# Performance work log

Measured on AMD Instinct MI355X. Metric: run time of the kernel, lower is better.

## Reference

```python
import jax, jax.numpy as jnp
import numpy as np

L, B, E = 2048, 4, 1024
H = 8
D1 = 2048          # expand_ratio * E, multiple of H
HD = D1 // H       # head dim 256
MAX_L = 2048
EPS = 1e-8


def setup_inputs() -> dict:
    key = jax.random.key(0)
    ks = jax.random.split(key, 9)
    std = 0.02
    return {
        "x": jax.random.normal(ks[0], (L, B, E), jnp.float32),
        "Wu": jax.random.normal(ks[1], (D1, E), jnp.float32) * std,
        "bu": jax.random.normal(ks[2], (D1,), jnp.float32) * std,
        "Wv": jax.random.normal(ks[3], (D1, E), jnp.float32) * std,
        "bv": jax.random.normal(ks[4], (D1,), jnp.float32) * std,
        "Wo": jax.random.normal(ks[5], (E, D1), jnp.float32) * std,
        "bo": jax.random.normal(ks[6], (E,), jnp.float32) * std,
        "zero": jax.random.normal(ks[7], (H, 1), jnp.float32) * 0.1,   # Toeplitz coef, offset 0
        "pos": jax.random.normal(ks[8], (H, MAX_L - 1), jnp.float32) * 0.1,  # offsets 1..n-1
    }


def _simple_rmsnorm(x):
    d = x.shape[-1]
    rms = jnp.linalg.norm(x, axis=-1, keepdims=True) * (d ** -0.5)
    return x / (rms + EPS)


def _toeplitz_causal_fft(v, zero, pos):
    # v: (b, h, n, hd); causal Toeplitz mixing along n via FFT long conv
    n = v.shape[-2]
    coef = jnp.concatenate([zero, pos[:, : n - 1]], axis=-1)  # (h, n)
    m = 2 * n
    cf = jnp.fft.rfft(coef, m, axis=-1)                  # (h, m//2+1)
    vf = jnp.fft.rfft(v, m, axis=-2)                     # (b, h, m//2+1, hd)
    out = jnp.fft.irfft(cf[None, :, :, None] * vf, m, axis=-2)
    return out[:, :, :n, :]


def reference(x, Wu, bu, Wv, bv, Wo, bo, zero, pos):
    # x: (n, b, e) fairseq layout
    n, b, e = x.shape
    shortcut = x
    xn = _simple_rmsnorm(x)                               # pre_norm (SimpleRMSNorm, no params)
    u = jax.nn.silu(jnp.einsum('nbe,de->nbd', xn, Wu) + bu)   # (n,b,d1)
    v = jax.nn.silu(jnp.einsum('nbe,de->nbd', xn, Wv) + bv)   # (n,b,d1)
    # 'n b (h d) -> b h n d'
    vh = v.transpose(1, 0, 2).reshape(b, n, H, HD).transpose(0, 2, 1, 3)
    oh = _toeplitz_causal_fft(vh, zero, pos)              # (b,h,n,hd)
    o = oh.transpose(0, 2, 1, 3).reshape(b, n, D1).transpose(1, 0, 2)  # (n,b,d1)
    o = u * o                                             # gating
    out = jnp.einsum('nbd,ed->nbe', o, Wo) + bo + shortcut
    return out
```

## Files before the change

### kernel.cpp

```cpp
#include <hip/hip_runtime.h>
#include <cstdint>
#include <cstddef>

#define LQ   2048
#define BQ   4
#define EQ   1024
#define HQ   8
#define D1Q  2048
#define HDQ  256
#define NBQ  (LQ*BQ)

typedef __bf16 bf16_t;
typedef __bf16 bf16x8 __attribute__((ext_vector_type(8)));
typedef __bf16 bf16x4 __attribute__((ext_vector_type(4)));
typedef float  f32x4  __attribute__((ext_vector_type(4)));

#define GAS1(p) ((const __attribute__((address_space(1))) void*)(p))
#define LAS3(p) ((__attribute__((address_space(3))) void*)(p))


__global__ __launch_bounds__(256) void convert_kernel(
    const float* __restrict__ Wu, const float* __restrict__ Wv,
    const float* __restrict__ Wo,
    bf16_t* __restrict__ Wub, bf16_t* __restrict__ Wvb,
    bf16_t* __restrict__ Wob)
{
    const size_t i = (size_t)blockIdx.x * 256 + threadIdx.x;
    if (i < (size_t)D1Q * EQ) {
        Wub[i] = (bf16_t)Wu[i];
        Wvb[i] = (bf16_t)Wv[i];
        Wob[i] = (bf16_t)Wo[i];
    }
}

__global__ __launch_bounds__(256) void build_toep_tiles(
    const float* __restrict__ zero, const float* __restrict__ pos,
    bf16_t* __restrict__ Atiles)
{
    const int q = blockIdx.x;
    const int h = blockIdx.y;
    const int doff = (q - 3) * 32;
    const int tid = threadIdx.x;
    bf16_t* dst = Atiles + ((size_t)h * 64 + q) * (128 * 32);
    const int e0 = tid * 16;
    const int r = e0 >> 5;
    const int cbase = e0 & 31;
    bf16_t vals[16];
    #pragma unroll
    for (int j = 0; j < 16; ++j) {
        const int d = doff + r - (cbase + j);
        float v = 0.f;
        if (d == 0) v = zero[h];
        else if (d > 0) v = pos[(size_t)h * (LQ - 1) + d - 1];
        vals[j] = (bf16_t)v;
    }
    *(bf16x8*)(dst + e0)     = *(bf16x8*)(vals);
    *(bf16x8*)(dst + e0 + 8) = *(bf16x8*)(vals + 8);
}

__global__ __launch_bounds__(256) void rmsnorm_kernel(
    const float* __restrict__ x, bf16_t* __restrict__ xn)
{
    const int row = blockIdx.x;
    const int tid = threadIdx.x;
    const float4 v = ((const float4*)(x + (size_t)row * EQ))[tid];
    float ss = v.x*v.x + v.y*v.y + v.z*v.z + v.w*v.w;
    #pragma unroll
    for (int m = 32; m >= 1; m >>= 1) ss += __shfl_xor(ss, m, 64);
    __shared__ float red[4];
    const int wid = tid >> 6, lane = tid & 63;
    if (lane == 0) red[wid] = ss;
    __syncthreads();
    const float tot = red[0] + red[1] + red[2] + red[3];
    const float inv = 1.f / (sqrtf(tot * (1.f / EQ)) + 1e-8f);
    bf16x4 o;
    o[0] = (bf16_t)(v.x * inv); o[1] = (bf16_t)(v.y * inv);
    o[2] = (bf16_t)(v.z * inv); o[3] = (bf16_t)(v.w * inv);
    *(bf16x4*)(xn + (size_t)row * EQ + tid * 4) = o;
}


template<int NREP, int MODE>
__global__ __launch_bounds__(512, 1) void gemm8p(
    const bf16_t* __restrict__ A, const bf16_t* __restrict__ Bm,
    int K, int N,
    const float* __restrict__ bias, const float* __restrict__ res,
    bf16_t* __restrict__ Cb, float* __restrict__ Cf)
{
    constexpr int LB      = NREP / 2;
    constexpr int BSTRIDE = 16384 + NREP * 4096;
    __shared__ alignas(16) char smem[3 * BSTRIDE];

    const int nwg   = gridDim.x * gridDim.y;
    const int bid   = blockIdx.y * gridDim.x + blockIdx.x;
    const int chunkw = nwg >> 3;
    const int sb    = (bid & 7) * chunkw + (bid >> 3);
    const int bx    = sb % gridDim.x;
    const int by    = sb / gridDim.x;

    const int tid  = threadIdx.x;
    const int wid  = tid >> 6;
    const int lane = tid & 63;
    const int frow = lane & 15;
    const int c    = lane >> 4;
    const int m0 = by * 256;
    const int n0 = bx * (NREP * 64);
    const int wrm = (wid >> 2) * 128;
    const int wrn = (wid & 3) * (NREP * 16);

    const int Ra = wrm + frow;
    const int ga = (Ra ^ (Ra >> 2)) & 3;
    const int offA = Ra * 64 + ((c ^ ga) << 4);
    const int Rb = wrn + frow;
    const int gb = (Rb ^ (Rb >> 2)) & 3;
    const int offB = 16384 + Rb * 64 + ((c ^ gb) << 4);

    const int sr   = tid >> 2;
    const int slot = tid & 3;
    const int gs   = (sr ^ (sr >> 2)) & 3;
    const size_t lda = (size_t)K * 2;
    const char* srcA  = (const char*)A  + (size_t)(m0 + sr) * lda + ((slot ^ gs) << 4);
    const char* srcA2 = srcA + 128 * lda;
    const char* srcB  = (const char*)Bm + (size_t)(n0 + sr) * lda + ((slot ^ gs) << 4);
    const char* srcB2 = srcB + 128 * lda;

    auto STAGE_A = [&](int buf, int kt) {
        char* d = smem + buf * BSTRIDE + wid * 1024;
        __builtin_amdgcn_global_load_lds(GAS1(srcA  + (size_t)kt * 64), LAS3(d), 16, 0, 0);
        __builtin_amdgcn_global_load_lds(GAS1(srcA2 + (size_t)kt * 64), LAS3(d + 8192), 16, 0, 0);
    };
    auto STAGE_B = [&](int buf, int kt) {
        char* d = smem + buf * BSTRIDE + 16384 + wid * 1024;
        __builtin_amdgcn_global_load_lds(GAS1(srcB  + (size_t)kt * 64), LAS3(d), 16, 0, 0);
        if constexpr (LB == 2)
            __builtin_amdgcn_global_load_lds(GAS1(srcB2 + (size_t)kt * 64), LAS3(d + 8192), 16, 0, 0);
    };

    f32x4 acc[8][NREP];
    #pragma unroll
    for (int i = 0; i < 8; ++i)
        #pragma unroll
        for (int j = 0; j < NREP; ++j) acc[i][j] = (f32x4){0.f, 0.f, 0.f, 0.f};

    const int NT = K >> 5;

    STAGE_A(0, 0); STAGE_B(0, 0);
    STAGE_A(1, 1); STAGE_B(1, 1);
    if constexpr (LB == 2) asm volatile("s_waitcnt vmcnt(4)" ::: "memory");
    else                   asm volatile("s_waitcnt vmcnt(3)" ::: "memory");
    __builtin_amdgcn_s_barrier();

    int buf = 0;
    for (int kq = 0; kq < NT; ++kq) {
        const char* base = smem + buf * BSTRIDE;
        int pbuf = buf + 2; if (pbuf >= 3) pbuf -= 3;
        const bool pf = (kq < NT - 2);

        bf16x8 av[4], bv[NREP];
        #pragma unroll
        for (int i = 0; i < 4; ++i)
            av[i] = *(const bf16x8*)(base + offA + i * 1024);
        #pragma unroll
        for (int i = 0; i < NREP; ++i)
            bv[i] = *(const bf16x8*)(base + offB + i * 1024);
        if (pf) STAGE_A(pbuf, kq + 2);
        __builtin_amdgcn_s_barrier();
        __builtin_amdgcn_s_setprio(1);
        #pragma unroll
        for (int mi = 0; mi < 4; ++mi)
            #pragma unroll
            for (int ni = 0; ni < NREP; ++ni)
                acc[mi][ni] = __builtin_amdgcn_mfma_f32_16x16x32_bf16(
                    av[mi], bv[ni], acc[mi][ni], 0, 0, 0);
        __builtin_amdgcn_s_setprio(0);
        __builtin_amdgcn_sched_barrier(0);
        __builtin_amdgcn_s_barrier();

        #pragma unroll
        for (int i = 0; i < 4; ++i)
            av[i] = *(const bf16x8*)(base + offA + (4 + i) * 1024);
        if (pf) STAGE_B(pbuf, kq + 2);
        __builtin_amdgcn_s_barrier();
        __builtin_amdgcn_s_setprio(1);
        #pragma unroll
        for (int mi = 0; mi < 4; ++mi)
            #pragma unroll
            for (int ni = 0; ni < NREP; ++ni)
                acc[4 + mi][ni] = __builtin_amdgcn_mfma_f32_16x16x32_bf16(
                    av[mi], bv[ni], acc[4 + mi][ni], 0, 0, 0);
        __builtin_amdgcn_s_setprio(0);
        __builtin_amdgcn_sched_barrier(0);

        if (kq < NT - 1) {
            if (kq <= NT - 3) {
                if constexpr (LB == 2) asm volatile("s_waitcnt vmcnt(4)" ::: "memory");
                else                   asm volatile("s_waitcnt vmcnt(3)" ::: "memory");
            } else {
                asm volatile("s_waitcnt vmcnt(0)" ::: "memory");
            }
            __builtin_amdgcn_s_barrier();
        }
        buf = (buf == 2) ? 0 : buf + 1;
    }

    if constexpr (MODE == 1) {
        static_assert(NREP == 4, "MODE 1 requires NREP=4");
        const int hh = n0 >> 8;
        float bb[4];
        #pragma unroll
        for (int ni = 0; ni < 4; ++ni) bb[ni] = bias[n0 + wrn + ni * 16 + frow];

        #pragma unroll
        for (int p = 0; p < 2; ++p) {
            __syncthreads();
            bf16_t* chunk = (bf16_t*)smem + wid * 4608;
            #pragma unroll
            for (int mi2 = 0; mi2 < 4; ++mi2) {
                #pragma unroll
                for (int ni = 0; ni < 4; ++ni) {
                    const int nl = ni * 16 + frow;
                    #pragma unroll
                    for (int j = 0; j < 4; ++j) {
                        float v = acc[p * 4 + mi2][ni][j] + bb[ni];
                        v = v / (1.f + __expf(-v));
                        chunk[nl * 72 + j * 16 + mi2 * 4 + c] = (bf16_t)v;
                    }
                }
            }
            __syncthreads();
            const int hd = wrn + lane;
            const int tb = (m0 + wrm + p * 64) >> 2;
            const bf16_t* rowp = chunk + lane * 72;
            #pragma unroll
            for (int b2 = 0; b2 < 4; ++b2) {
                bf16x8 r0 = *(const bf16x8*)(rowp + b2 * 16);
                bf16x8 r1 = *(const bf16x8*)(rowp + b2 * 16 + 8);
                bf16_t* dst = Cb + (((size_t)hh * 4 + b2) * 256 + hd) * (size_t)LQ + tb;
                *(bf16x8*)(dst)     = r0;
                *(bf16x8*)(dst + 8) = r1;
            }
        }
        return;
    }

    const int fq = c * 4;
    #pragma unroll
    for (int mi = 0; mi < 8; ++mi) {
        #pragma unroll
        for (int ni = 0; ni < NREP; ++ni) {
            const int gn = n0 + wrn + ni * 16 + frow;
            #pragma unroll
            for (int j = 0; j < 4; ++j) {
                const int gm = m0 + wrm + mi * 16 + fq + j;
                float v = acc[mi][ni][j];
                if constexpr (MODE == 0) {
                    v += bias[gn];
                    v = v / (1.f + __expf(-v));
                    Cb[(size_t)gm * N + gn] = (bf16_t)v;
                } else {
                    v += bias[gn] + res[(size_t)gm * N + gn];
                    Cf[(size_t)gm * N + gn] = v;
                }
            }
        }
    }
}

__global__ __launch_bounds__(512, 4) void gemm_toep8p(
    const bf16_t* __restrict__ VT, const bf16_t* __restrict__ Atiles,
    const bf16_t* __restrict__ U, bf16_t* __restrict__ O)
{
    constexpr int BSTRIDE = 24576;
    __shared__ alignas(16) char smem[3 * BSTRIDE];

    const int bid   = blockIdx.x;
    const int m_blk = 15 - (bid >> 5);
    const int sub   = bid & 31;
    const int h     = sub >> 2;
    const int n0    = (sub & 3) * 256;
    const int m0    = m_blk * 128;

    const int tid  = threadIdx.x;
    const int wid  = tid >> 6;
    const int lane = tid & 63;
    const int frow = lane & 15;
    const int c    = lane >> 4;
    const int wrm  = (wid >> 2) * 64;
    const int wrn  = (wid & 3) * 64;

    const int Ra = wrm + frow;
    const int ga = (Ra ^ (Ra >> 2)) & 3;
    const int offA = Ra * 64 + ((c ^ ga) << 4);
    const int Rb = wrn + frow;
    const int gb = (Rb ^ (Rb >> 2)) & 3;
    const int offB = 8192 + Rb * 64 + ((c ^ gb) << 4);

    const int sr   = tid >> 2;
    const int slot = tid & 3;
    const int gs   = (sr ^ (sr >> 2)) & 3;
    const int soff = (slot ^ gs) << 4;

    const char* Ah = (const char*)(Atiles + (size_t)h * 64 * 4096);
    const size_t ldb = (size_t)LQ * 2;
    const char* srcB  = (const char*)VT + ((size_t)h * 1024 + n0 + sr) * ldb + soff;
    const char* srcB2 = srcB + 128 * ldb;

    auto STAGE_A = [&](int buf, int kt) {
        const int q = 4 * m_blk + 3 - kt;
        const char* s = Ah + (size_t)q * 8192 + (size_t)sr * 64 + soff;
        __builtin_amdgcn_global_load_lds(GAS1(s),
                                         LAS3(smem + buf * BSTRIDE + wid * 1024), 16, 0, 0);
    };
    auto STAGE_B = [&](int buf, int kt) {
        char* d = smem + buf * BSTRIDE + 8192 + wid * 1024;
        __builtin_amdgcn_global_load_lds(GAS1(srcB  + (size_t)kt * 64), LAS3(d), 16, 0, 0);
        __builtin_amdgcn_global_load_lds(GAS1(srcB2 + (size_t)kt * 64), LAS3(d + 8192), 16, 0, 0);
    };

    f32x4 acc[4][4];
    #pragma unroll
    for (int i = 0; i < 4; ++i)
        #pragma unroll
        for (int j = 0; j < 4; ++j) acc[i][j] = (f32x4){0.f, 0.f, 0.f, 0.f};

    const int NT = 4 * m_blk + 4;

    STAGE_A(0, 0); STAGE_B(0, 0);
    STAGE_A(1, 1); STAGE_B(1, 1);
    asm volatile("s_waitcnt vmcnt(3)" ::: "memory");
    __builtin_amdgcn_s_barrier();

    int buf = 0;
    for (int kq = 0; kq < NT; ++kq) {
        const char* base = smem + buf * BSTRIDE;
        int pbuf = buf + 2; if (pbuf >= 3) pbuf -= 3;
        const bool pf = (kq < NT - 2);

        bf16x8 av[4], bv[4];
        #pragma unroll
        for (int i = 0; i < 4; ++i)
            av[i] = *(const bf16x8*)(base + offA + i * 1024);
        #pragma unroll
        for (int i = 0; i < 2; ++i)
            bv[i] = *(const bf16x8*)(base + offB + i * 1024);
        if (pf) STAGE_A(pbuf, kq + 2);
        __builtin_amdgcn_s_barrier();
        __builtin_amdgcn_s_setprio(1);
        #pragma unroll
        for (int mi = 0; mi < 4; ++mi)
            #pragma unroll
            for (int ni = 0; ni < 2; ++ni)
                acc[mi][ni] = __builtin_amdgcn_mfma_f32_16x16x32_bf16(
                    av[mi], bv[ni], acc[mi][ni], 0, 0, 0);
        __builtin_amdgcn_s_setprio(0);
        __builtin_amdgcn_sched_barrier(0);
        __builtin_amdgcn_s_barrier();

        #pragma unroll
        for (int i = 2; i < 4; ++i)
            bv[i] = *(const bf16x8*)(base + offB + i * 1024);
        if (pf) STAGE_B(pbuf, kq + 2);
        __builtin_amdgcn_s_barrier();
        __builtin_amdgcn_s_setprio(1);
        #pragma unroll
        for (int mi = 0; mi < 4; ++mi)
            #pragma unroll
            for (int ni = 2; ni < 4; ++ni)
                acc[mi][ni] = __builtin_amdgcn_mfma_f32_16x16x32_bf16(
                    av[mi], bv[ni], acc[mi][ni], 0, 0, 0);
        __builtin_amdgcn_s_setprio(0);
        __builtin_amdgcn_sched_barrier(0);

        if (kq < NT - 1) {
            if (kq <= NT - 3) asm volatile("s_waitcnt vmcnt(3)" ::: "memory");
            else              asm volatile("s_waitcnt vmcnt(0)" ::: "memory");
            __builtin_amdgcn_s_barrier();
        }
        buf = (buf == 2) ? 0 : buf + 1;
    }

    const int fq = c * 4;
    #pragma unroll
    for (int mi = 0; mi < 4; ++mi) {
        #pragma unroll
        for (int ni = 0; ni < 4; ++ni) {
            const int nn = n0 + wrn + ni * 16 + frow;
            const int b  = nn >> 8, hd = nn & 255;
            #pragma unroll
            for (int j = 0; j < 4; ++j) {
                const int t = m0 + wrm + mi * 16 + fq + j;
                const size_t idx = ((size_t)t * BQ + b) * D1Q + h * HDQ + hd;
                const float uval = (float)U[idx];
                O[idx] = (bf16_t)(uval * acc[mi][ni][j]);
            }
        }
    }
}


extern "C" void kernel_launch(void* const* d_in, const int* in_sizes, int n_in,
                              void* d_out, int out_size, void* d_ws, size_t ws_size,
                              hipStream_t stream)
{
    const float* x    = (const float*)d_in[0];
    const float* Wu   = (const float*)d_in[1];
    const float* bu   = (const float*)d_in[2];
    const float* Wv   = (const float*)d_in[3];
    const float* bv   = (const float*)d_in[4];
    const float* Wo   = (const float*)d_in[5];
    const float* bo   = (const float*)d_in[6];
    const float* zero = (const float*)d_in[7];
    const float* pos  = (const float*)d_in[8];
    float* out = (float*)d_out;

    char* ws = (char*)d_ws;
    size_t off = 0;
    auto alloc = [&](size_t bytes) {
        char* p = ws + off;
        off += (bytes + 255) & ~(size_t)255;
        return p;
    };
    bf16_t* xn     = (bf16_t*)alloc((size_t)NBQ * EQ * 2);
    bf16_t* Wub    = (bf16_t*)alloc((size_t)D1Q * EQ * 2);
    bf16_t* Wvb    = (bf16_t*)alloc((size_t)D1Q * EQ * 2);
    bf16_t* Wob    = (bf16_t*)alloc((size_t)EQ * D1Q * 2);
    bf16_t* Atiles = (bf16_t*)alloc((size_t)HQ * 64 * 4096 * 2);
    bf16_t* Ub     = (bf16_t*)alloc((size_t)NBQ * D1Q * 2);
    bf16_t* VTb    = (bf16_t*)alloc((size_t)NBQ * D1Q * 2);
    bf16_t* Ob     = (bf16_t*)alloc((size_t)NBQ * D1Q * 2);

    convert_kernel<<<8192, 256, 0, stream>>>(Wu, Wv, Wo, Wub, Wvb, Wob);
    build_toep_tiles<<<dim3(64, 8), 256, 0, stream>>>(zero, pos, Atiles);
    rmsnorm_kernel<<<NBQ, 256, 0, stream>>>(x, xn);

    dim3 g1(D1Q / 256, NBQ / 256);
    gemm8p<4, 0><<<g1, 512, 0, stream>>>(xn, Wub, EQ, D1Q, bu, nullptr, Ub, nullptr);
    gemm8p<4, 1><<<g1, 512, 0, stream>>>(xn, Wvb, EQ, D1Q, bv, nullptr, VTb, nullptr);

    gemm_toep8p<<<512, 512, 0, stream>>>(VTb, Atiles, Ub, Ob);

    dim3 g2(EQ / 128, NBQ / 256);
    gemm8p<2, 2><<<g2, 512, 0, stream>>>(Ob, Wob, D1Q, EQ, bo, x, nullptr, out);
}
```

Before: 225.6 us.

## Restructure GEMM pipeline to double-buffered BK=64 with templated warp geometry

Reworks the dense GEMM kernel from a triple-buffered BK=32 pipeline to a double-buffered BK=64 pipeline with an 8-way XOR swizzle and 128-byte rows. Warp tiling becomes a template (MI, WM, WN), and launch bounds are raised to allow two workgroups per CU. The transposed-store epilogue is rewritten for the new tile layout. The aim is fewer barriers per unit of K and better latency hiding through occupancy. The cost is a shallower prefetch distance and more registers per workgroup. It also drops the sched_barrier calls in the Toeplitz GEMM.

Result: faster. 208.5 us (-7.6%).

```diff
diff --git a/kernel.cpp b/kernel.cpp
--- a/kernel.cpp
+++ b/kernel.cpp
@@ -80,16 +80,24 @@
 }
 
 
-template<int NREP, int MODE>
-__global__ __launch_bounds__(512, 1) void gemm8p(
+template<int MI, int WM, int WN, int MODE>
+__global__ __launch_bounds__(512, 2) void gemm8p(
     const bf16_t* __restrict__ A, const bf16_t* __restrict__ Bm,
     int K, int N,
     const float* __restrict__ bias, const float* __restrict__ res,
     bf16_t* __restrict__ Cb, float* __restrict__ Cf)
 {
-    constexpr int LB      = NREP / 2;
-    constexpr int BSTRIDE = 16384 + NREP * 4096;
-    __shared__ alignas(16) char smem[3 * BSTRIDE];
+    constexpr int BM = WM * MI * 16;
+    constexpr int BN = WN * 64;
+    constexpr int ABYTES = BM * 128;
+    constexpr int BBYTES = BN * 128;
+    constexpr int BSTRIDE = ABYTES + BBYTES;
+    constexpr int CA = BM / 64;
+    constexpr int CB = BN / 64;
+    constexpr int NPH = 2 * (MI / 4);
+    static_assert(BM == 256, "staging assumes BM=256");
+    static_assert(MODE != 1 || (MI == 8 && WN == 4), "MODE1 geometry");
+    __shared__ alignas(16) char smem[2 * BSTRIDE];
 
     const int nwg   = gridDim.x * gridDim.y;
     const int bid   = blockIdx.y * gridDim.x + blockIdx.x;
@@ -103,108 +111,97 @@
     const int lane = tid & 63;
     const int frow = lane & 15;
     const int c    = lane >> 4;
-    const int m0 = by * 256;
-    const int n0 = bx * (NREP * 64);
-    const int wrm = (wid >> 2) * 128;
-    const int wrn = (wid & 3) * (NREP * 16);
-
-    const int Ra = wrm + frow;
-    const int ga = (Ra ^ (Ra >> 2)) & 3;
-    const int offA = Ra * 64 + ((c ^ ga) << 4);
-    const int Rb = wrn + frow;
-    const int gb = (Rb ^ (Rb >> 2)) & 3;
-    const int offB = 16384 + Rb * 64 + ((c ^ gb) << 4);
-
-    const int sr   = tid >> 2;
-    const int slot = tid & 3;
-    const int gs   = (sr ^ (sr >> 2)) & 3;
-    const size_t lda = (size_t)K * 2;
-    const char* srcA  = (const char*)A  + (size_t)(m0 + sr) * lda + ((slot ^ gs) << 4);
-    const char* srcA2 = srcA + 128 * lda;
-    const char* srcB  = (const char*)Bm + (size_t)(n0 + sr) * lda + ((slot ^ gs) << 4);
-    const char* srcB2 = srcB + 128 * lda;
-
-    auto STAGE_A = [&](int buf, int kt) {
-        char* d = smem + buf * BSTRIDE + wid * 1024;
-        __builtin_amdgcn_global_load_lds(GAS1(srcA  + (size_t)kt * 64), LAS3(d), 16, 0, 0);
-        __builtin_amdgcn_global_load_lds(GAS1(srcA2 + (size_t)kt * 64), LAS3(d + 8192), 16, 0, 0);
+    const int m0 = by * BM;
+    const int n0 = bx * BN;
+    const int wm = wid / WN, wn = wid % WN;
+    const int wrm = wm * (MI * 16);
+    const int wrn = wn * 64;
+
+    const int g = frow & 7;
+    const int offA0 = (wrm + frow) * 128 + ((c ^ g) << 4);
+    const int offA1 = offA0 ^ 64;
+    const int offB0 = (wrn + frow) * 128 + ((c ^ g) << 4);
+    const int offB1 = offB0 ^ 64;
+
+    const int rl = tid >> 3;
+    const int ps = tid & 7;
+    const int ls = ps ^ (rl & 7);
+    const size_t lda2 = (size_t)K * 2;
+    const char* sA = (const char*)A  + (size_t)(m0 + rl) * lda2 + ls * 16;
+    const char* sB = (const char*)Bm + (size_t)(n0 + rl) * lda2 + ls * 16;
+
+    auto STAGE_A = [&](int bf, int kt) {
+        char* d = smem + bf * BSTRIDE + wid * 1024;
+        #pragma unroll
+        for (int cl = 0; cl < CA; ++cl)
+            __builtin_amdgcn_global_load_lds(
+                GAS1(sA + (size_t)cl * 64 * lda2 + (size_t)kt * 128),
+                LAS3(d + cl * 8192), 16, 0, 0);
     };
-    auto STAGE_B = [&](int buf, int kt) {
-        char* d = smem + buf * BSTRIDE + 16384 + wid * 1024;
-        __builtin_amdgcn_global_load_lds(GAS1(srcB  + (size_t)kt * 64), LAS3(d), 16, 0, 0);
-        if constexpr (LB == 2)
-            __builtin_amdgcn_global_load_lds(GAS1(srcB2 + (size_t)kt * 64), LAS3(d + 8192), 16, 0, 0);
+    auto STAGE_B = [&](int bf, int kt) {
+        char* d = smem + bf * BSTRIDE + ABYTES + wid * 1024;
+        #pragma unroll
+        for (int cl = 0; cl < CB; ++cl)
+            __builtin_amdgcn_global_load_lds(
+                GAS1(sB + (size_t)cl * 64 * lda2 + (size_t)kt * 128),
+                LAS3(d + cl * 8192), 16, 0, 0);
     };
 
-    f32x4 acc[8][NREP];
-    #pragma unroll
-    for (int i = 0; i < 8; ++i)
-        #pragma unroll
-        for (int j = 0; j < NREP; ++j) acc[i][j] = (f32x4){0.f, 0.f, 0.f, 0.f};
-
-    const int NT = K >> 5;
+    f32x4 acc[MI][4];
+    #pragma unroll
+    for (int i = 0; i < MI; ++i)
+        #pragma unroll
+        for (int j = 0; j < 4; ++j) acc[i][j] = (f32x4){0.f, 0.f, 0.f, 0.f};
+
+    const int NT = K >> 6;
 
     STAGE_A(0, 0); STAGE_B(0, 0);
-    STAGE_A(1, 1); STAGE_B(1, 1);
-    if constexpr (LB == 2) asm volatile("s_waitcnt vmcnt(4)" ::: "memory");
-    else                   asm volatile("s_waitcnt vmcnt(3)" ::: "memory");
+    asm volatile("s_waitcnt vmcnt(0)" ::: "memory");
     __builtin_amdgcn_s_barrier();
 
     int buf = 0;
-    for (int kq = 0; kq < NT; ++kq) {
-        const char* base = smem + buf * BSTRIDE;
-        int pbuf = buf + 2; if (pbuf >= 3) pbuf -= 3;
-        const bool pf = (kq < NT - 2);
-
-        bf16x8 av[4], bv[NREP];
-        #pragma unroll
-        for (int i = 0; i < 4; ++i)
-            av[i] = *(const bf16x8*)(base + offA + i * 1024);
-        #pragma unroll
-        for (int i = 0; i < NREP; ++i)
-            bv[i] = *(const bf16x8*)(base + offB + i * 1024);
-        if (pf) STAGE_A(pbuf, kq + 2);
-        __builtin_amdgcn_s_barrier();
-        __builtin_amdgcn_s_setprio(1);
-        #pragma unroll
-        for (int mi = 0; mi < 4; ++mi)
-            #pragma unroll
-            for (int ni = 0; ni < NREP; ++ni)
-                acc[mi][ni] = __builtin_amdgcn_mfma_f32_16x16x32_bf16(
-                    av[mi], bv[ni], acc[mi][ni], 0, 0, 0);
-        __builtin_amdgcn_s_setprio(0);
-        __builtin_amdgcn_sched_barrier(0);
-        __builtin_amdgcn_s_barrier();
-
-        #pragma unroll
-        for (int i = 0; i < 4; ++i)
-            av[i] = *(const bf16x8*)(base + offA + (4 + i) * 1024);
-        if (pf) STAGE_B(pbuf, kq + 2);
-        __builtin_amdgcn_s_barrier();
-        __builtin_amdgcn_s_setprio(1);
-        #pragma unroll
-        for (int mi = 0; mi < 4; ++mi)
-            #pragma unroll
-            for (int ni = 0; ni < NREP; ++ni)
-                acc[4 + mi][ni] = __builtin_amdgcn_mfma_f32_16x16x32_bf16(
-                    av[mi], bv[ni], acc[4 + mi][ni], 0, 0, 0);
-        __builtin_amdgcn_s_setprio(0);
-        __builtin_amdgcn_sched_barrier(0);
-
-        if (kq < NT - 1) {
-            if (kq <= NT - 3) {
-                if constexpr (LB == 2) asm volatile("s_waitcnt vmcnt(4)" ::: "memory");
-                else                   asm volatile("s_waitcnt vmcnt(3)" ::: "memory");
-            } else {
-                asm volatile("s_waitcnt vmcnt(0)" ::: "memory");
+    for (int t = 0; t < NT; ++t) {
+        const char* bA = smem + buf * BSTRIDE;
+        const char* bB = bA + ABYTES;
+        const bool pf = (t + 1 < NT);
+        const int nb = buf ^ 1;
+        bf16x8 av[4], bv[4];
+
+        #pragma unroll
+        for (int kk = 0; kk < 2; ++kk) {
+            #pragma unroll
+            for (int mh = 0; mh < MI / 4; ++mh) {
+                constexpr int MH = MI / 4;
+                const int p = kk * MH + mh;
+                #pragma unroll
+                for (int i = 0; i < 4; ++i)
+                    av[i] = *(const bf16x8*)(bA + (mh * 4 + i) * 2048 + (kk ? offA1 : offA0));
+                if (mh == 0) {
+                    #pragma unroll
+                    for (int i = 0; i < 4; ++i)
+                        bv[i] = *(const bf16x8*)(bB + i * 2048 + (kk ? offB1 : offB0));
+                }
+                if (pf && p == 0) STAGE_A(nb, t + 1);
+                if (pf && p == 1) STAGE_B(nb, t + 1);
+                __builtin_amdgcn_s_barrier();
+                __builtin_amdgcn_s_setprio(1);
+                #pragma unroll
+                for (int i = 0; i < 4; ++i)
+                    #pragma unroll
+                    for (int ni = 0; ni < 4; ++ni)
+                        acc[mh * 4 + i][ni] = __builtin_amdgcn_mfma_f32_16x16x32_bf16(
+                            av[i], bv[ni], acc[mh * 4 + i][ni], 0, 0, 0);
+                __builtin_amdgcn_s_setprio(0);
+                if (p == NPH - 1) {
+                    if (pf) asm volatile("s_waitcnt vmcnt(0)" ::: "memory");
+                }
+                __builtin_amdgcn_s_barrier();
             }
-            __builtin_amdgcn_s_barrier();
         }
-        buf = (buf == 2) ? 0 : buf + 1;
+        buf ^= 1;
     }
 
     if constexpr (MODE == 1) {
-        static_assert(NREP == 4, "MODE 1 requires NREP=4");
         const int hh = n0 >> 8;
         float bb[4];
         #pragma unroll
@@ -213,31 +210,34 @@
         #pragma unroll
         for (int p = 0; p < 2; ++p) {
             __syncthreads();
-            bf16_t* chunk = (bf16_t*)smem + wid * 4608;
-            #pragma unroll
-            for (int mi2 = 0; mi2 < 4; ++mi2) {
+            bf16_t* chunk = (bf16_t*)smem + wid * 4224;
+            #pragma unroll
+            for (int mi = 0; mi < 8; ++mi) {
                 #pragma unroll
-                for (int ni = 0; ni < 4; ++ni) {
-                    const int nl = ni * 16 + frow;
+                for (int nio = 0; nio < 2; ++nio) {
+                    const int ni = p * 2 + nio;
+                    const int nl = nio * 16 + frow;
                     #pragma unroll
                     for (int j = 0; j < 4; ++j) {
-                        float v = acc[p * 4 + mi2][ni][j] + bb[ni];
+                        float v = acc[mi][ni][j] + bb[ni];
                         v = v / (1.f + __expf(-v));
-                        chunk[nl * 72 + j * 16 + mi2 * 4 + c] = (bf16_t)v;
+                        chunk[nl * 132 + j * 32 + mi * 4 + c] = (bf16_t)v;
                     }
                 }
             }
             __syncthreads();
-            const int hd = wrn + lane;
-            const int tb = (m0 + wrm + p * 64) >> 2;
-            const bf16_t* rowp = chunk + lane * 72;
-            #pragma unroll
-            for (int b2 = 0; b2 < 4; ++b2) {
-                bf16x8 r0 = *(const bf16x8*)(rowp + b2 * 16);
-                bf16x8 r1 = *(const bf16x8*)(rowp + b2 * 16 + 8);
-                bf16_t* dst = Cb + (((size_t)hh * 4 + b2) * 256 + hd) * (size_t)LQ + tb;
-                *(bf16x8*)(dst)     = r0;
-                *(bf16x8*)(dst + 8) = r1;
+            const int nl  = lane & 31;
+            const int bh2 = lane >> 5;
+            const int hd  = wrn + p * 32 + nl;
+            const int t0  = (m0 + wrm) >> 2;
+            #pragma unroll
+            for (int bi = 0; bi < 2; ++bi) {
+                const int b2 = bh2 * 2 + bi;
+                const bf16_t* src = chunk + nl * 132 + b2 * 32;
+                bf16_t* dst = Cb + (((size_t)hh * 4 + b2) * 256 + hd) * (size_t)LQ + t0;
+                #pragma unroll
+                for (int q = 0; q < 4; ++q)
+                    *(bf16x8*)(dst + q * 8) = *(const bf16x8*)(src + q * 8);
             }
         }
         return;
@@ -245,9 +245,9 @@
 
     const int fq = c * 4;
     #pragma unroll
-    for (int mi = 0; mi < 8; ++mi) {
-        #pragma unroll
-        for (int ni = 0; ni < NREP; ++ni) {
+    for (int mi = 0; mi < MI; ++mi) {
+        #pragma unroll
+        for (int ni = 0; ni < 4; ++ni) {
             const int gn = n0 + wrn + ni * 16 + frow;
             #pragma unroll
             for (int j = 0; j < 4; ++j) {
@@ -353,7 +353,6 @@
                 acc[mi][ni] = __builtin_amdgcn_mfma_f32_16x16x32_bf16(
                     av[mi], bv[ni], acc[mi][ni], 0, 0, 0);
         __builtin_amdgcn_s_setprio(0);
-        __builtin_amdgcn_sched_barrier(0);
         __builtin_amdgcn_s_barrier();
 
         #pragma unroll
@@ -369,7 +368,6 @@
                 acc[mi][ni] = __builtin_amdgcn_mfma_f32_16x16x32_bf16(
                     av[mi], bv[ni], acc[mi][ni], 0, 0, 0);
         __builtin_amdgcn_s_setprio(0);
-        __builtin_amdgcn_sched_barrier(0);
 
         if (kq < NT - 1) {
             if (kq <= NT - 3) asm volatile("s_waitcnt vmcnt(3)" ::: "memory");
@@ -434,11 +432,11 @@
     rmsnorm_kernel<<<NBQ, 256, 0, stream>>>(x, xn);
 
     dim3 g1(D1Q / 256, NBQ / 256);
-    gemm8p<4, 0><<<g1, 512, 0, stream>>>(xn, Wub, EQ, D1Q, bu, nullptr, Ub, nullptr);
-    gemm8p<4, 1><<<g1, 512, 0, stream>>>(xn, Wvb, EQ, D1Q, bv, nullptr, VTb, nullptr);
+    gemm8p<8, 2, 4, 0><<<g1, 512, 0, stream>>>(xn, Wub, EQ, D1Q, bu, nullptr, Ub, nullptr);
+    gemm8p<8, 2, 4, 1><<<g1, 512, 0, stream>>>(xn, Wvb, EQ, D1Q, bv, nullptr, VTb, nullptr);
 
     gemm_toep8p<<<512, 512, 0, stream>>>(VTb, Atiles, Ub, Ob);
 
     dim3 g2(EQ / 128, NBQ / 256);
-    gemm8p<2, 2><<<g2, 512, 0, stream>>>(Ob, Wob, D1Q, EQ, bo, x, nullptr, out);
-}
+    gemm8p<4, 4, 2, 2><<<g2, 512, 0, stream>>>(Ob, Wob, D1Q, EQ, bo, x, nullptr, out);
+}
```
